# Kernel optimization log

Hardware: AMD Instinct MI355X
Metric: run time of the kernel (lower is better)

Reference implementation:

```python
import jax, jax.numpy as jnp
import numpy as np

B, N, FIN, H, D = 4, 2048, 128, 4, 64
ALPHA = 0.2  # LeakyReLU negative slope


def _xavier_uniform(key, shape):
    fan_in, fan_out = shape[0], shape[1]
    limit = float(np.sqrt(6.0 / (fan_in + fan_out)))
    return jax.random.uniform(key, shape, jnp.float32, -limit, limit)


def setup_inputs() -> dict:
    key = jax.random.key(0)
    k1, k2, k3, k4 = jax.random.split(key, 4)
    x = jax.random.normal(k1, (B, N, FIN), jnp.float32)
    adj = jax.random.randint(k2, (B, N, N), 0, 2, jnp.int32)  # dense 0/1 mask
    W = _xavier_uniform(k3, (FIN, H * D))
    a = _xavier_uniform(k4, (2 * D, 1))
    return {"x": x, "adj": adj, "W": W, "a": a}


def reference(x, adj, W, a):
    Bb, Nn, _ = x.shape
    Dd = a.shape[0] // 2
    Hh = W.shape[1] // Dd
    # h: [B, N, H, D]
    h = (x @ W).reshape(Bb, Nn, Hh, Dd)
    # Additive attention: e[b,i,j,h] = leakyrelu(a1 . h[b,i,h] + a2 . h[b,j,h])
    a1 = a[:Dd, 0]
    a2 = a[Dd:, 0]
    ei = jnp.einsum('bnhd,d->bnh', h, a1)  # source (row i) term
    ej = jnp.einsum('bnhd,d->bnh', h, a2)  # dest (col j) term
    e = ei[:, :, None, :] + ej[:, None, :, :]  # [B, N, N, H]
    e = jnp.where(e >= 0, e, ALPHA * e)  # LeakyReLU
    e = jnp.where(adj[..., None] == 0, -jnp.inf, e)
    att = jax.nn.softmax(e, axis=2)  # softmax over neighbors j
    # dropout is a no-op in eval mode (training=False)
    out = jnp.einsum('bijh,bjhd->bihd', att, h)  # [B, N, H, D]
    return out.mean(axis=2)  # mean over heads -> [B, N, D]
```

## Files before the change

### kernel.cpp

```cpp
#include <hip/hip_runtime.h>

#define NN 2048
#define NH 4
#define DD 64
#define FIN 128
#define NB 4
#define LOG2E 1.44269504f

typedef unsigned short u16;
typedef unsigned int u32;
typedef short sh8 __attribute__((ext_vector_type(8)));
typedef float f32x4 __attribute__((ext_vector_type(4)));

static __device__ __forceinline__ u16 f2bf(float f) {
    u32 u = __builtin_bit_cast(u32, f);
    u += 0x7fffu + ((u >> 16) & 1u);
    return (u16)(u >> 16);
}
static __device__ __forceinline__ u32 pk_bf(float a, float b) {
    u32 ua = __builtin_bit_cast(u32, a) + 0x8000u;
    u32 ub = __builtin_bit_cast(u32, b) + 0x8000u;
    return __builtin_amdgcn_perm(ub, ua, 0x07060302u);
}
static __device__ __forceinline__ u32 cvt_pk(float a, float b) {
    u32 r;
    asm("v_cvt_pk_bf16_f32 %0, %1, %2" : "=v"(r) : "v"(a), "v"(b));
    return r;
}
static __device__ __forceinline__ float fast_exp2(float x) {
    float r;
    asm("v_exp_f32 %0, %1" : "=v"(r) : "v"(x));
    return r;
}

static __device__ __forceinline__ void cd_probe(int ln15, int q, int* irow, int* icol) {
    sh8 pa, pb, qa, qb;
    #pragma unroll
    for (int ii = 0; ii < 8; ++ii) {
        pa[ii] = (short)f2bf((float)ln15);
        pb[ii] = 0;
        qa[ii] = 0;
        qb[ii] = (short)f2bf((float)ln15);
    }
    if (q == 0) { pb[0] = (short)f2bf(1.0f); qa[0] = (short)f2bf(1.0f); }
    f32x4 z = {};
    f32x4 prow = __builtin_amdgcn_mfma_f32_16x16x32_bf16(pa, pb, z, 0, 0, 0);
    f32x4 pcol = __builtin_amdgcn_mfma_f32_16x16x32_bf16(qa, qb, z, 0, 0, 0);
    #pragma unroll
    for (int r = 0; r < 4; ++r) {
        irow[r] = (int)(prow[r] + 0.5f);
        icol[r] = (int)(pcol[r] + 0.5f);
    }
}


__global__ __launch_bounds__(256)
void k_prep(const float* __restrict__ W, u16* __restrict__ WT) {
    const int bt  = blockIdx.x;
    const int kt  = bt & 3;
    const int ct8 = bt >> 2;
    __shared__ float tile[32][33];
    const int tid = threadIdx.x;
    const int rr = tid >> 5, cc = tid & 31;
    #pragma unroll
    for (int i = 0; i < 4; ++i)
        tile[rr + 8 * i][cc] = W[(size_t)(kt * 32 + rr + 8 * i) * 256 + ct8 * 32 + cc];
    __syncthreads();
    #pragma unroll
    for (int i = 0; i < 4; ++i)
        WT[(size_t)(ct8 * 32 + rr + 8 * i) * FIN + kt * 32 + cc] = f2bf(tile[cc][rr + 8 * i]);
}

__global__ __launch_bounds__(256)
void k_gemm_h(const float* __restrict__ x, const u16* __restrict__ WT,
              const float* __restrict__ a,
              u16* __restrict__ hTf, float* __restrict__ ei_g, float* __restrict__ ej_g) {
    const int nb = blockIdx.x, b = blockIdx.y;
    const int tid = threadIdx.x, hd = tid >> 6, lane = tid & 63, ln15 = lane & 15, q = lane >> 4;
    const int q8 = q * 8;
    const int n0 = nb * 64;

    __shared__ u16 xs[64][136];
    __shared__ float cs[NH][4][16][20];
    {
        const int col = (tid & 31) * 4;
        const int r0  = tid >> 5;
        #pragma unroll
        for (int rr = 0; rr < 8; ++rr) {
            const int row = r0 + rr * 8;
            const float4 v = *(const float4*)(x + ((size_t)(b * NN + n0 + row)) * FIN + col);
            *(u32*)&xs[row][col]     = pk_bf(v.x, v.y);
            *(u32*)&xs[row][col + 2] = pk_bf(v.z, v.w);
        }
    }
    __syncthreads();

    int irow[4], icol[4];
    cd_probe(ln15, q, irow, icol);

    f32x4 acc[4][4] = {};
    #pragma unroll
    for (int ks = 0; ks < 4; ++ks) {
        sh8 af[4], bfr[4];
        #pragma unroll
        for (int ct = 0; ct < 4; ++ct)
            af[ct] = *(const sh8*)(WT + (size_t)(hd * 64 + ct * 16 + ln15) * FIN + ks * 32 + q8);
        #pragma unroll
        for (int nt = 0; nt < 4; ++nt)
            bfr[nt] = *(const sh8*)&xs[nt * 16 + ln15][ks * 32 + q8];
        #pragma unroll
        for (int ct = 0; ct < 4; ++ct)
            #pragma unroll
            for (int nt = 0; nt < 4; ++nt)
                acc[ct][nt] = __builtin_amdgcn_mfma_f32_16x16x32_bf16(af[ct], bfr[nt], acc[ct][nt], 0, 0, 0);
    }

    float eip[4] = {}, ejq[4] = {};
    #pragma unroll
    for (int ct = 0; ct < 4; ++ct) {
        #pragma unroll
        for (int nt = 0; nt < 4; ++nt)
            #pragma unroll
            for (int r = 0; r < 4; ++r)
                cs[hd][nt][irow[r]][icol[r]] = acc[ct][nt][r];

        #pragma unroll
        for (int p = 0; p < 2; ++p) {
            const float4 c0 = *(const float4*)&cs[hd][2 * p + (q >> 1)][ln15][(q & 1) * 8];
            const float4 c1 = *(const float4*)&cs[hd][2 * p + (q >> 1)][ln15][(q & 1) * 8 + 4];
            uint4 o;
            o.x = pk_bf(c0.x, c0.y); o.y = pk_bf(c0.z, c0.w);
            o.z = pk_bf(c1.x, c1.y); o.w = pk_bf(c1.z, c1.w);
            *(uint4*)(hTf + ((((size_t)(b * NH + hd) * 64 + nb * 2 + p) * 4 + ct) * 512) + lane * 8) = o;
        }

        float a1v[4], a2v[4];
        #pragma unroll
        for (int r = 0; r < 4; ++r) {
            const int d = ct * 16 + 4 * q + r;
            a1v[r] = a[d] * LOG2E;
            a2v[r] = a[64 + d] * LOG2E;
        }
        #pragma unroll
        for (int nt = 0; nt < 4; ++nt)
            #pragma unroll
            for (int r = 0; r < 4; ++r) {
                const float v = cs[hd][nt][4 * q + r][ln15];
                eip[nt] += v * a1v[r];
                ejq[nt] += v * a2v[r];
            }
    }
    #pragma unroll
    for (int nt = 0; nt < 4; ++nt) {
        eip[nt] += __shfl_xor(eip[nt], 16);
        eip[nt] += __shfl_xor(eip[nt], 32);
        ejq[nt] += __shfl_xor(ejq[nt], 16);
        ejq[nt] += __shfl_xor(ejq[nt], 32);
    }
    if (lane < 16) {
        const size_t bhd = (size_t)(b * NH + hd) * NN;
        #pragma unroll
        for (int nt = 0; nt < 4; ++nt) {
            ei_g[bhd + n0 + nt * 16 + lane] = eip[nt];
            ej_g[bhd + n0 + nt * 16 + lane] = ejq[nt];
        }
    }
}

template <int NJT>
__global__ __launch_bounds__(256, 4)
void k_attn(const int* __restrict__ adj, const u16* __restrict__ hTf,
            const float* __restrict__ ei_g, const float* __restrict__ ej_g,
            float* __restrict__ o_part, float* __restrict__ l_part) {
    const int ib = blockIdx.x, js = blockIdx.y, b = blockIdx.z;
    const int js_n = gridDim.y;
    const int tid = threadIdx.x, hd = tid >> 6, lane = tid & 63, ln15 = lane & 15, q = lane >> 4;
    const int q8 = q * 8;
    const int iA = ib * 32 + ln15;
    const int jt0 = js * NJT;

    __shared__ u32 mlds[32][NJT + 1];
    __shared__ float ejs[NH][NJT * 32];

    {
        const int row = (hd << 3) + (lane >> 3);
        const int* abase = adj + (size_t)(b * NN + ib * 32 + row) * NN + jt0 * 32 + (lane & 7) * 4;
        #pragma unroll
        for (int jb = 0; jb < NJT; jb += 8) {
            int4 vv[8];
            #pragma unroll
            for (int u = 0; u < 8; ++u)
                vv[u] = *(const int4*)(abase + (jb + u) * 32);
            #pragma unroll
            for (int u = 0; u < 8; ++u) {
                u32 nib = (vv[u].x ? 1u : 0u) | (vv[u].y ? 2u : 0u) |
                          (vv[u].z ? 4u : 0u) | (vv[u].w ? 8u : 0u);
                u32 w = nib << (4 * (lane & 7));
                w |= __shfl_xor(w, 1);
                w |= __shfl_xor(w, 2);
                w |= __shfl_xor(w, 4);
                if ((lane & 7) == 0) mlds[row][jb + u] = w;
            }
        }
    }
    const size_t bhd = (size_t)(b * NH + hd) * NN;
    {
        const float* src = ej_g + bhd + jt0 * 32;
        #pragma unroll
        for (int u = 0; u < NJT / 8; ++u) {
            const int o4 = (u * 64 + lane) * 4;
            *(float4*)&ejs[hd][o4] = *(const float4*)(src + o4);
        }
    }
    __syncthreads();

    int irow[4], icol[4];
    cd_probe(ln15, q, irow, icol);

    const float eivA = ei_g[bhd + iA];
    const float eivB = ei_g[bhd + iA + 16];
    const u16*  hfp  = hTf + (size_t)(b * NH + hd) * (64 * 2048) + (size_t)lane * 8;

    sh8 ones;
    #pragma unroll
    for (int ii = 0; ii < 8; ++ii) ones[ii] = (short)0x3F80;

    f32x4 acc[8] = {};
    f32x4 accl[2] = {};

    auto COMPUTE = [&](int t, uint4& oA, uint4& oB) {
        const u32 mA = mlds[ln15][t];
        const u32 mB = mlds[ln15 + 16][t];
        const float4 e0 = *(const float4*)&ejs[hd][t * 32 + q8];
        const float4 e1 = *(const float4*)&ejs[hd][t * 32 + q8 + 4];
        const float ef[8] = { e0.x, e0.y, e0.z, e0.w, e1.x, e1.y, e1.z, e1.w };
        const u32 mqA = mA >> q8;
        const u32 mqB = mB >> q8;
        float pA[8], pB[8];
        #pragma unroll
        for (int ii = 0; ii < 8; ++ii) {
            float eA = eivA + ef[ii];
            float eB = eivB + ef[ii];
            eA = fmaxf(eA, 0.2f * eA);
            eB = fmaxf(eB, 0.2f * eB);
            const float xA = fast_exp2(eA);
            const float xB = fast_exp2(eB);
            pA[ii] = (mqA & (1u << ii)) ? xA : 0.f;
            pB[ii] = (mqB & (1u << ii)) ? xB : 0.f;
        }
        oA.x = cvt_pk(pA[0], pA[1]); oA.y = cvt_pk(pA[2], pA[3]);
        oA.z = cvt_pk(pA[4], pA[5]); oA.w = cvt_pk(pA[6], pA[7]);
        oB.x = cvt_pk(pB[0], pB[1]); oB.y = cvt_pk(pB[2], pB[3]);
        oB.z = cvt_pk(pB[4], pB[5]); oB.w = cvt_pk(pB[6], pB[7]);
    };

    sh8 H[2][4];
    #pragma unroll
    for (int s = 0; s < 2; ++s)
        #pragma unroll
        for (int k = 0; k < 4; ++k)
            H[s][k] = *(const sh8*)(hfp + (size_t)(jt0 + s) * 2048 + k * 512);

    uint4 avAc, avBc, avAn, avBn;
    COMPUTE(0, avAc, avBc);

    #pragma unroll
    for (int t = 0; t < NJT; ++t) {
        if (t + 1 < NJT) COMPUTE(t + 1, avAn, avBn);

        const sh8 av = __builtin_bit_cast(sh8, avAc);
        const sh8 bv = __builtin_bit_cast(sh8, avBc);
        acc[0] = __builtin_amdgcn_mfma_f32_16x16x32_bf16(av, H[t & 1][0], acc[0], 0, 0, 0);
        acc[1] = __builtin_amdgcn_mfma_f32_16x16x32_bf16(av, H[t & 1][1], acc[1], 0, 0, 0);
        acc[2] = __builtin_amdgcn_mfma_f32_16x16x32_bf16(av, H[t & 1][2], acc[2], 0, 0, 0);
        acc[3] = __builtin_amdgcn_mfma_f32_16x16x32_bf16(av, H[t & 1][3], acc[3], 0, 0, 0);
        accl[0] = __builtin_amdgcn_mfma_f32_16x16x32_bf16(av, ones, accl[0], 0, 0, 0);
        acc[4] = __builtin_amdgcn_mfma_f32_16x16x32_bf16(bv, H[t & 1][0], acc[4], 0, 0, 0);
        acc[5] = __builtin_amdgcn_mfma_f32_16x16x32_bf16(bv, H[t & 1][1], acc[5], 0, 0, 0);
        acc[6] = __builtin_amdgcn_mfma_f32_16x16x32_bf16(bv, H[t & 1][2], acc[6], 0, 0, 0);
        acc[7] = __builtin_amdgcn_mfma_f32_16x16x32_bf16(bv, H[t & 1][3], acc[7], 0, 0, 0);
        accl[1] = __builtin_amdgcn_mfma_f32_16x16x32_bf16(bv, ones, accl[1], 0, 0, 0);

        if (t + 2 < NJT) {
            #pragma unroll
            for (int k = 0; k < 4; ++k)
                H[t & 1][k] = *(const sh8*)(hfp + (size_t)(jt0 + t + 2) * 2048 + k * 512);
        }
        if (t + 1 < NJT) { avAc = avAn; avBc = avBn; }
    }

    const size_t pbA = (((size_t)b * 128 + ib * 2 + 0) * js_n + js) * NH + hd;
    const size_t pbB = (((size_t)b * 128 + ib * 2 + 1) * js_n + js) * NH + hd;
    #pragma unroll
    for (int r = 0; r < 4; ++r) {
        l_part[pbA * 16 + irow[r]] = accl[0][r];
        l_part[pbB * 16 + irow[r]] = accl[1][r];
    }
    float* opA = o_part + pbA * 1024;
    float* opB = o_part + pbB * 1024;
    #pragma unroll
    for (int dt = 0; dt < 4; ++dt)
        #pragma unroll
        for (int r = 0; r < 4; ++r) {
            opA[(size_t)irow[r] * 64 + dt * 16 + icol[r]] = acc[dt][r];
            opB[(size_t)irow[r] * 64 + dt * 16 + icol[r]] = acc[4 + dt][r];
        }
}

template <int JS>
__global__ __launch_bounds__(256)
void k_combine(const float* __restrict__ o_part, const float* __restrict__ l_part,
               float* __restrict__ out) {
    const int ib = blockIdx.x, b = blockIdx.y;
    const int tid = threadIdx.x;
    const int i = tid >> 4, d4 = (tid & 15) * 4;
    float4 sacc = {0.f, 0.f, 0.f, 0.f};
    #pragma unroll
    for (int h = 0; h < NH; ++h) {
        float l = 0.f;
        float4 oh = {0.f, 0.f, 0.f, 0.f};
        #pragma unroll
        for (int js = 0; js < JS; ++js) {
            const size_t pbase = (((size_t)b * 128 + ib) * JS + js) * NH + h;
            l += l_part[pbase * 16 + i];
            const float4 ov = *(const float4*)(o_part + pbase * 1024 + (size_t)i * 64 + d4);
            oh.x += ov.x; oh.y += ov.y; oh.z += ov.z; oh.w += ov.w;
        }
        const float inv = 0.25f / l;
        sacc.x += oh.x * inv; sacc.y += oh.y * inv;
        sacc.z += oh.z * inv; sacc.w += oh.w * inv;
    }
    *(float4*)(out + ((size_t)(b * NN) + ib * 16 + i) * DD + d4) = sacc;
}

extern "C" void kernel_launch(void* const* d_in, const int* in_sizes, int n_in,
                              void* d_out, int out_size, void* d_ws, size_t ws_size,
                              hipStream_t stream) {
    const float* x = nullptr; const int* adj = nullptr;
    const float* W = nullptr; const float* a = nullptr;
    for (int i = 0; i < n_in; ++i) {
        switch (in_sizes[i]) {
            case NB * NN * FIN:  x   = (const float*)d_in[i]; break;
            case NB * NN * NN:   adj = (const int*)d_in[i];   break;
            case FIN * 256:      W   = (const float*)d_in[i]; break;
            case 2 * DD:         a   = (const float*)d_in[i]; break;
            default: break;
        }
    }
    if (!x)   x   = (const float*)d_in[0];
    if (!adj) adj = (const int*)d_in[1];
    if (!W)   W   = (const float*)d_in[2];
    if (!a)   a   = (const float*)d_in[3];
    float* out = (float*)d_out;

    char* ws = (char*)d_ws;
    u16*   WT  = (u16*)(ws);
    float* ei  = (float*)(ws + 65536);
    float* ej  = (float*)(ws + 196608);
    u16*   hTf = (u16*)(ws + 327680);
    float* l_p = (float*)(ws + 6619136);
    float* o_p = (float*)(ws + 7143424);

    const size_t need4 = 7143424 + (size_t)4 * 8388608;
    const size_t need2 = 7143424 + (size_t)2 * 8388608;
    const int js_n = (ws_size >= need4) ? 4 : (ws_size >= need2) ? 2 : 1;

    k_prep<<<dim3(32), dim3(256), 0, stream>>>(W, WT);
    k_gemm_h<<<dim3(32, NB), dim3(256), 0, stream>>>(x, WT, a, hTf, ei, ej);
    if (js_n == 4)
        k_attn<16><<<dim3(64, 4, NB), dim3(256), 0, stream>>>(adj, hTf, ei, ej, o_p, l_p);
    else if (js_n == 2)
        k_attn<32><<<dim3(64, 2, NB), dim3(256), 0, stream>>>(adj, hTf, ei, ej, o_p, l_p);
    else
        k_attn<64><<<dim3(64, 1, NB), dim3(256), 0, stream>>>(adj, hTf, ei, ej, o_p, l_p);
    if (js_n == 4)      k_combine<4><<<dim3(128, NB), dim3(256), 0, stream>>>(o_p, l_p, out);
    else if (js_n == 2) k_combine<2><<<dim3(128, NB), dim3(256), 0, stream>>>(o_p, l_p, out);
    else                k_combine<1><<<dim3(128, NB), dim3(256), 0, stream>>>(o_p, l_p, out);
}
```

Before: 136.3 us.

## Factor leaky-ReLU exponent into per-node exp2 products, removing exp from attention loop

Because exp2 is monotone, exp2(leaky(ei+ej)) equals max(exp2(ei)*exp2(ej), exp2(0.2ei)*exp2(0.2ej)). The GEMM kernel now precomputes four per-node exponential arrays, so the attention inner loop needs only multiplies and a max instead of transcendental exps. The adjacency mask is also stored expanded to 16-bit all-ones/zero lanes in LDS, so it can be applied with a bitwise AND after bf16 packing. The change also drops the single-split fallback and lowers the occupancy hint from 4 to 3. The trade-offs are larger LDS usage, extra global arrays, and slightly different rounding from multiplying exponentials.

```diff
diff --git a/kernel.cpp b/kernel.cpp
--- a/kernel.cpp
+++ b/kernel.cpp
@@ -74,7 +74,8 @@
 __global__ __launch_bounds__(256)
 void k_gemm_h(const float* __restrict__ x, const u16* __restrict__ WT,
               const float* __restrict__ a,
-              u16* __restrict__ hTf, float* __restrict__ ei_g, float* __restrict__ ej_g) {
+              u16* __restrict__ hTf, float* __restrict__ Ea_g, float* __restrict__ Ga_g,
+              float* __restrict__ Fb_g, float* __restrict__ Hb_g) {
     const int nb = blockIdx.x, b = blockIdx.y;
     const int tid = threadIdx.x, hd = tid >> 6, lane = tid & 63, ln15 = lane & 15, q = lane >> 4;
     const int q8 = q * 8;
@@ -161,16 +162,20 @@
         const size_t bhd = (size_t)(b * NH + hd) * NN;
         #pragma unroll
         for (int nt = 0; nt < 4; ++nt) {
-            ei_g[bhd + n0 + nt * 16 + lane] = eip[nt];
-            ej_g[bhd + n0 + nt * 16 + lane] = ejq[nt];
+            const size_t idx = bhd + n0 + nt * 16 + lane;
+            Ea_g[idx] = fast_exp2(eip[nt]);
+            Ga_g[idx] = fast_exp2(0.2f * eip[nt]);
+            Fb_g[idx] = fast_exp2(ejq[nt]);
+            Hb_g[idx] = fast_exp2(0.2f * ejq[nt]);
         }
     }
 }
 
 template <int NJT>
-__global__ __launch_bounds__(256, 4)
+__global__ __launch_bounds__(256, 3)
 void k_attn(const int* __restrict__ adj, const u16* __restrict__ hTf,
-            const float* __restrict__ ei_g, const float* __restrict__ ej_g,
+            const float* __restrict__ Ea, const float* __restrict__ Ga,
+            const float* __restrict__ Fb, const float* __restrict__ Hb,
             float* __restrict__ o_part, float* __restrict__ l_part) {
     const int ib = blockIdx.x, js = blockIdx.y, b = blockIdx.z;
     const int js_n = gridDim.y;
@@ -179,12 +184,14 @@
     const int iA = ib * 32 + ln15;
     const int jt0 = js * NJT;
 
-    __shared__ u32 mlds[32][NJT + 1];
-    __shared__ float ejs[NH][NJT * 32];
+    __shared__ u32   pmsk[32][NJT * 16 + 4];
+    __shared__ float fjs[NH][NJT * 32];
+    __shared__ float hjs[NH][NJT * 32];
 
     {
         const int row = (hd << 3) + (lane >> 3);
-        const int* abase = adj + (size_t)(b * NN + ib * 32 + row) * NN + jt0 * 32 + (lane & 7) * 4;
+        const int lk = lane & 7;
+        const int* abase = adj + (size_t)(b * NN + ib * 32 + row) * NN + jt0 * 32 + lk * 4;
         #pragma unroll
         for (int jb = 0; jb < NJT; jb += 8) {
             int4 vv[8];
@@ -193,23 +200,22 @@
                 vv[u] = *(const int4*)(abase + (jb + u) * 32);
             #pragma unroll
             for (int u = 0; u < 8; ++u) {
-                u32 nib = (vv[u].x ? 1u : 0u) | (vv[u].y ? 2u : 0u) |
-                          (vv[u].z ? 4u : 0u) | (vv[u].w ? 8u : 0u);
-                u32 w = nib << (4 * (lane & 7));
-                w |= __shfl_xor(w, 1);
-                w |= __shfl_xor(w, 2);
-                w |= __shfl_xor(w, 4);
-                if ((lane & 7) == 0) mlds[row][jb + u] = w;
+                uint2 wv;
+                wv.x = (vv[u].x ? 0xFFFFu : 0u) | (vv[u].y ? 0xFFFF0000u : 0u);
+                wv.y = (vv[u].z ? 0xFFFFu : 0u) | (vv[u].w ? 0xFFFF0000u : 0u);
+                *(uint2*)&pmsk[row][(jb + u) * 16 + lk * 2] = wv;
             }
         }
     }
     const size_t bhd = (size_t)(b * NH + hd) * NN;
     {
-        const float* src = ej_g + bhd + jt0 * 32;
+        const float* fsrc = Fb + bhd + jt0 * 32;
+        const float* hsrc = Hb + bhd + jt0 * 32;
         #pragma unroll
         for (int u = 0; u < NJT / 8; ++u) {
             const int o4 = (u * 64 + lane) * 4;
-            *(float4*)&ejs[hd][o4] = *(const float4*)(src + o4);
+            *(float4*)&fjs[hd][o4] = *(const float4*)(fsrc + o4);
+            *(float4*)&hjs[hd][o4] = *(const float4*)(hsrc + o4);
         }
     }
     __syncthreads();
@@ -217,9 +223,11 @@
     int irow[4], icol[4];
     cd_probe(ln15, q, irow, icol);
 
-    const float eivA = ei_g[bhd + iA];
-    const float eivB = ei_g[bhd + iA + 16];
-    const u16*  hfp  = hTf + (size_t)(b * NH + hd) * (64 * 2048) + (size_t)lane * 8;
+    const float EiA = Ea[bhd + iA];
+    const float GiA = Ga[bhd + iA];
+    const float EiB = Ea[bhd + iA + 16];
+    const float GiB = Ga[bhd + iA + 16];
+    const u16*  hfp = hTf + (size_t)(b * NH + hd) * (64 * 2048) + (size_t)lane * 8;
 
     sh8 ones;
     #pragma unroll
@@ -228,32 +236,6 @@
     f32x4 acc[8] = {};
     f32x4 accl[2] = {};
 
-    auto COMPUTE = [&](int t, uint4& oA, uint4& oB) {
-        const u32 mA = mlds[ln15][t];
-        const u32 mB = mlds[ln15 + 16][t];
-        const float4 e0 = *(const float4*)&ejs[hd][t * 32 + q8];
-        const float4 e1 = *(const float4*)&ejs[hd][t * 32 + q8 + 4];
-        const float ef[8] = { e0.x, e0.y, e0.z, e0.w, e1.x, e1.y, e1.z, e1.w };
-        const u32 mqA = mA >> q8;
-        const u32 mqB = mB >> q8;
-        float pA[8], pB[8];
-        #pragma unroll
-        for (int ii = 0; ii < 8; ++ii) {
-            float eA = eivA + ef[ii];
-            float eB = eivB + ef[ii];
-            eA = fmaxf(eA, 0.2f * eA);
-            eB = fmaxf(eB, 0.2f * eB);
-            const float xA = fast_exp2(eA);
-            const float xB = fast_exp2(eB);
-            pA[ii] = (mqA & (1u << ii)) ? xA : 0.f;
-            pB[ii] = (mqB & (1u << ii)) ? xB : 0.f;
-        }
-        oA.x = cvt_pk(pA[0], pA[1]); oA.y = cvt_pk(pA[2], pA[3]);
-        oA.z = cvt_pk(pA[4], pA[5]); oA.w = cvt_pk(pA[6], pA[7]);
-        oB.x = cvt_pk(pB[0], pB[1]); oB.y = cvt_pk(pB[2], pB[3]);
-        oB.z = cvt_pk(pB[4], pB[5]); oB.w = cvt_pk(pB[6], pB[7]);
-    };
-
     sh8 H[2][4];
     #pragma unroll
     for (int s = 0; s < 2; ++s)
@@ -261,15 +243,35 @@
         for (int k = 0; k < 4; ++k)
             H[s][k] = *(const sh8*)(hfp + (size_t)(jt0 + s) * 2048 + k * 512);
 
-    uint4 avAc, avBc, avAn, avBn;
-    COMPUTE(0, avAc, avBc);
-
     #pragma unroll
     for (int t = 0; t < NJT; ++t) {
-        if (t + 1 < NJT) COMPUTE(t + 1, avAn, avBn);
-
-        const sh8 av = __builtin_bit_cast(sh8, avAc);
-        const sh8 bv = __builtin_bit_cast(sh8, avBc);
+        const uint4 mwA = *(const uint4*)&pmsk[ln15][t * 16 + q * 4];
+        const uint4 mwB = *(const uint4*)&pmsk[ln15 + 16][t * 16 + q * 4];
+        const float4 f0 = *(const float4*)&fjs[hd][t * 32 + q8];
+        const float4 f1 = *(const float4*)&fjs[hd][t * 32 + q8 + 4];
+        const float4 h0 = *(const float4*)&hjs[hd][t * 32 + q8];
+        const float4 h1 = *(const float4*)&hjs[hd][t * 32 + q8 + 4];
+        const float pf[8] = { f0.x, f0.y, f0.z, f0.w, f1.x, f1.y, f1.z, f1.w };
+        const float ph[8] = { h0.x, h0.y, h0.z, h0.w, h1.x, h1.y, h1.z, h1.w };
+        const u32 mA[4] = { mwA.x, mwA.y, mwA.z, mwA.w };
+        const u32 mB[4] = { mwB.x, mwB.y, mwB.z, mwB.w };
+
+        uint4 uA, uB;
+        u32 wA[4], wB[4];
+        #pragma unroll
+        for (int p = 0; p < 4; ++p) {
+            const float a0 = fmaxf(EiA * pf[2 * p], GiA * ph[2 * p]);
+            const float a1 = fmaxf(EiA * pf[2 * p + 1], GiA * ph[2 * p + 1]);
+            wA[p] = cvt_pk(a0, a1) & mA[p];
+            const float b0 = fmaxf(EiB * pf[2 * p], GiB * ph[2 * p]);
+            const float b1 = fmaxf(EiB * pf[2 * p + 1], GiB * ph[2 * p + 1]);
+            wB[p] = cvt_pk(b0, b1) & mB[p];
+        }
+        uA.x = wA[0]; uA.y = wA[1]; uA.z = wA[2]; uA.w = wA[3];
+        uB.x = wB[0]; uB.y = wB[1]; uB.z = wB[2]; uB.w = wB[3];
+        const sh8 av = __builtin_bit_cast(sh8, uA);
+        const sh8 bv = __builtin_bit_cast(sh8, uB);
+
         acc[0] = __builtin_amdgcn_mfma_f32_16x16x32_bf16(av, H[t & 1][0], acc[0], 0, 0, 0);
         acc[1] = __builtin_amdgcn_mfma_f32_16x16x32_bf16(av, H[t & 1][1], acc[1], 0, 0, 0);
         acc[2] = __builtin_amdgcn_mfma_f32_16x16x32_bf16(av, H[t & 1][2], acc[2], 0, 0, 0);
@@ -286,7 +288,6 @@
             for (int k = 0; k < 4; ++k)
                 H[t & 1][k] = *(const sh8*)(hfp + (size_t)(jt0 + t + 2) * 2048 + k * 512);
         }
-        if (t + 1 < NJT) { avAc = avAn; avBc = avBn; }
     }
 
     const size_t pbA = (((size_t)b * 128 + ib * 2 + 0) * js_n + js) * NH + hd;
@@ -355,25 +356,23 @@
 
     char* ws = (char*)d_ws;
     u16*   WT  = (u16*)(ws);
-    float* ei  = (float*)(ws + 65536);
-    float* ej  = (float*)(ws + 196608);
-    u16*   hTf = (u16*)(ws + 327680);
-    float* l_p = (float*)(ws + 6619136);
-    float* o_p = (float*)(ws + 7143424);
-
-    const size_t need4 = 7143424 + (size_t)4 * 8388608;
-    const size_t need2 = 7143424 + (size_t)2 * 8388608;
-    const int js_n = (ws_size >= need4) ? 4 : (ws_size >= need2) ? 2 : 1;
+    float* Ea  = (float*)(ws + 65536);
+    float* Ga  = (float*)(ws + 196608);
+    float* Fb  = (float*)(ws + 327680);
+    float* Hb  = (float*)(ws + 458752);
+    u16*   hTf = (u16*)(ws + 589824);
+    float* l_p = (float*)(ws + 4784128);
+    float* o_p = (float*)(ws + 5308416);
+
+    const size_t need4 = 5308416 + (size_t)4 * 8388608;
+    const int js_n = (ws_size >= need4) ? 4 : 2;
 
     k_prep<<<dim3(32), dim3(256), 0, stream>>>(W, WT);
-    k_gemm_h<<<dim3(32, NB), dim3(256), 0, stream>>>(x, WT, a, hTf, ei, ej);
+    k_gemm_h<<<dim3(32, NB), dim3(256), 0, stream>>>(x, WT, a, hTf, Ea, Ga, Fb, Hb);
     if (js_n == 4)
-        k_attn<16><<<dim3(64, 4, NB), dim3(256), 0, stream>>>(adj, hTf, ei, ej, o_p, l_p);
-    else if (js_n == 2)
-        k_attn<32><<<dim3(64, 2, NB), dim3(256), 0, stream>>>(adj, hTf, ei, ej, o_p, l_p);
+        k_attn<16><<<dim3(64, 4, NB), dim3(256), 0, stream>>>(adj, hTf, Ea, Ga, Fb, Hb, o_p, l_p);
     else
-        k_attn<64><<<dim3(64, 1, NB), dim3(256), 0, stream>>>(adj, hTf, ei, ej, o_p, l_p);
+        k_attn<32><<<dim3(64, 2, NB), dim3(256), 0, stream>>>(adj, hTf, Ea, Ga, Fb, Hb, o_p, l_p);
     if (js_n == 4)      k_combine<4><<<dim3(128, NB), dim3(256), 0, stream>>>(o_p, l_p, out);
-    else if (js_n == 2) k_combine<2><<<dim3(128, NB), dim3(256), 0, stream>>>(o_p, l_p, out);
-    else                k_combine<1><<<dim3(128, NB), dim3(256), 0, stream>>>(o_p, l_p, out);
-}
+    else                k_combine<2><<<dim3(128, NB), dim3(256), 0, stream>>>(o_p, l_p, out);
+}
```

After: 134.6 us. No clear change (-1.2%).
